# Kernel tuning notes

Hardware: AMD Instinct MI355X
Metric: run time of the kernel (lower is better)

The kernel has to match this reference:

```python
import jax, jax.numpy as jnp
import numpy as np

N = 100000   # nodes
E = 3200000  # edges (avg degree 32)
D = 768      # embedding_dim (XLM-R)
H = 256      # hidden_dim
L = 3        # num GCN layers
C = 3        # verdict classes


def setup_inputs() -> dict:
    key = jax.random.key(0)
    ks = jax.random.split(key, 8)
    s = 0.02
    return dict(
        node_features=jax.random.normal(ks[0], (N, D), jnp.float32),
        edge_src=jax.random.randint(ks[1], (E,), 0, N),
        edge_dst=jax.random.randint(ks[2], (E,), 0, N),
        claim_node_idx=0,
        W_in=(jax.random.normal(ks[3], (D, H), jnp.float32) * s),
        b_in=jnp.zeros((H,), jnp.float32),
        W_gnn=(jax.random.normal(ks[4], (L, H, H), jnp.float32) * s),
        b_gnn=jnp.zeros((L, H), jnp.float32),
        Wc1=(jax.random.normal(ks[5], (H, H // 2), jnp.float32) * s),
        bc1=jnp.zeros((H // 2,), jnp.float32),
        Wc2=(jax.random.normal(ks[6], (H // 2, C), jnp.float32) * s),
        bc2=jnp.zeros((C,), jnp.float32),
    )


def reference(node_features, edge_src, edge_dst, claim_node_idx,
              W_in, b_in, W_gnn, b_gnn, Wc1, bc1, Wc2, bc2):
    n = node_features.shape[0]
    dt = node_features.dtype
    ones = jnp.ones((edge_src.shape[0],), dt)
    # DGL GraphConv norm='both': symmetric normalization, degrees clamped >= 1
    deg_out = jnp.clip(jax.ops.segment_sum(ones, edge_src, num_segments=n), 1.0)
    deg_in = jnp.clip(jax.ops.segment_sum(ones, edge_dst, num_segments=n), 1.0)
    norm_src = deg_out ** -0.5  # [n]
    norm_dst = deg_in ** -0.5   # [n]

    # input projection
    h = node_features @ W_in + b_in  # [n, H]

    # GCN layers: relu(D_dst^-1/2 A D_src^-1/2 (h) W + b); dropout is identity in eval
    for l in range(W_gnn.shape[0]):
        msg = (h * norm_src[:, None])[edge_src]                      # [E, H] gather
        agg = jax.ops.segment_sum(msg, edge_dst, num_segments=n)     # [n, H] scatter-add
        agg = agg * norm_dst[:, None]
        h = jax.nn.relu(agg @ W_gnn[l] + b_gnn[l])

    claim = h[claim_node_idx]                       # [H]
    hid = jax.nn.relu(claim @ Wc1 + bc1)            # [H//2]
    logits = hid @ Wc2 + bc2                        # [C]
    return logits
```

## Files before the change

kernel.cpp:

```cpp
#include <hip/hip_runtime.h>
#include <hip/hip_bf16.h>

#define D_IN 768
#define H_DIM 256
#define H_HALF 128
#define N_CLASSES 3

#define CAP1 256
#define CAP2 16384
#define CAPDEG 128
#define CAP0 1024

typedef __attribute__((ext_vector_type(8))) short bf16x8;
typedef __attribute__((ext_vector_type(4))) float f32x4;

static __device__ __forceinline__ unsigned short f2bf(float f) {
    union { float f; unsigned u; } x; x.f = f;
    unsigned u = x.u;
    return (unsigned short)((u + 0x7FFFu + ((u >> 16) & 1u)) >> 16);
}
static __device__ __forceinline__ float bf2f(unsigned short b) {
    union { unsigned u; float f; } x; x.u = ((unsigned)b) << 16;
    return x.f;
}
static __device__ __forceinline__ float bflo(unsigned v) {
    union { unsigned u; float f; } x; x.u = v << 16;
    return x.f;
}
static __device__ __forceinline__ float bfhi(unsigned v) {
    union { unsigned u; float f; } x; x.u = v & 0xFFFF0000u;
    return x.f;
}
static __device__ __forceinline__ bool bit_test(const unsigned* __restrict__ bm, int i) {
    return (bm[i >> 5] >> (i & 31)) & 1u;
}

static __device__ __forceinline__ void try_append(int s, int* __restrict__ pos,
                                                  int* __restrict__ list, int* __restrict__ cnt,
                                                  unsigned* __restrict__ bmCur,
                                                  unsigned* __restrict__ bmL) {
    if (atomicCAS(&pos[s], -1, -2) == -1) {
        int i = atomicAdd(cnt, 1);
        list[i] = s;
        atomicOr(&bmCur[s >> 5], 1u << (s & 31));
        atomicOr(&bmL[s >> 5], 1u << (s & 31));
        atomicExch(&pos[s], i);
    }
}

__global__ void k_pass1(const int* __restrict__ src, const int* __restrict__ dst,
                        const int* __restrict__ claim, int* __restrict__ B0,
                        int* __restrict__ cur0, int* __restrict__ pos1,
                        int* __restrict__ list1, int* __restrict__ cnt1,
                        unsigned* __restrict__ bm1, unsigned* __restrict__ bmL,
                        const float* __restrict__ W_in, const float* __restrict__ W_gnn,
                        unsigned short* __restrict__ Wth_in, unsigned short* __restrict__ Wtl_in,
                        unsigned short* __restrict__ Wth_g, unsigned short* __restrict__ Wtl_g,
                        int E) {
    int idx = blockIdx.x * 256 + threadIdx.x;
    int nth = gridDim.x * 256;
    {
        const int n1 = D_IN * H_DIM;
        const int ntot = n1 + 2 * H_DIM * H_DIM;
        for (int id = idx; id < ntot; id += nth) {
            if (id < n1) {
                int k = id >> 8, n = id & 255;
                float w = W_in[id];
                unsigned short h = f2bf(w);
                Wth_in[(size_t)n * D_IN + k] = h;
                Wtl_in[(size_t)n * D_IN + k] = f2bf(w - bf2f(h));
            } else {
                int t = id - n1;
                int l = t >> 16, r = t & 65535;
                int k = r >> 8, n = r & 255;
                float w = W_gnn[(size_t)l * 65536 + r];
                unsigned short h = f2bf(w);
                Wth_g[(size_t)l * 65536 + (size_t)n * H_DIM + k] = h;
                Wtl_g[(size_t)l * 65536 + (size_t)n * H_DIM + k] = f2bf(w - bf2f(h));
            }
        }
    }
    int c = claim[0];
    int e0 = idx * 4;
    if (e0 >= E) return;
    if (e0 + 4 <= E) {
        int4 d4 = *(const int4*)(dst + e0);
#pragma unroll
        for (int k = 0; k < 4; k++) {
            int d = (k == 0) ? d4.x : (k == 1) ? d4.y : (k == 2) ? d4.z : d4.w;
            if (d == c) {
                int s = src[e0 + k];
                int p = atomicAdd(cur0, 1);
                if (p < CAP0) B0[p] = s;
                try_append(s, pos1, list1, cnt1, bm1, bmL);
            }
        }
    } else {
        for (int e = e0; e < E; e++) {
            int d = dst[e];
            if (d == c) {
                int s = src[e];
                int p = atomicAdd(cur0, 1);
                if (p < CAP0) B0[p] = s;
                try_append(s, pos1, list1, cnt1, bm1, bmL);
            }
        }
    }
}

__global__ void k_scan_bm(const int* __restrict__ dst, const unsigned* __restrict__ bmPrev,
                          unsigned char* __restrict__ mb, int E) {
    int idx = blockIdx.x * 256 + threadIdx.x;
    int e0 = idx * 4;
    if (e0 >= E) return;
    unsigned m = 0;
    if (e0 + 4 <= E) {
        int4 d4 = *(const int4*)(dst + e0);
        m  = bit_test(bmPrev, d4.x) ? 1u : 0u;
        m |= bit_test(bmPrev, d4.y) ? 2u : 0u;
        m |= bit_test(bmPrev, d4.z) ? 4u : 0u;
        m |= bit_test(bmPrev, d4.w) ? 8u : 0u;
    } else {
        for (int e = e0; e < E; e++)
            if (bit_test(bmPrev, dst[e])) m |= 1u << (e - e0);
    }
    mb[idx] = (unsigned char)m;
}

__global__ void k_xexpand(const unsigned char* __restrict__ mb, int nbytes,
                          const int* __restrict__ src, const int* __restrict__ dst,
                          const int* __restrict__ posPrev, int* __restrict__ bucket,
                          int* __restrict__ cur, int* __restrict__ posCur,
                          int* __restrict__ listCur, int* __restrict__ cntCur,
                          unsigned* __restrict__ bmCur, unsigned* __restrict__ bmL) {
    int i = blockIdx.x * 256 + threadIdx.x;
    int nwords = (nbytes + 3) / 4;
    if (i >= nwords) return;
    unsigned w = *(const unsigned*)(mb + (size_t)i * 4);
    int rem = nbytes - i * 4;
    if (rem < 4) w &= (1u << (rem * 8)) - 1u;
    if (!w) return;
    while (w) {
        int b = __ffs(w) - 1;
        w &= w - 1;
        int e = (i * 4 + (b >> 3)) * 4 + (b & 7);
        int s = src[e], d = dst[e];
        int pt = posPrev[d];
        int p = atomicAdd(&cur[pt], 1);
        if (p < CAPDEG) bucket[(size_t)pt * CAPDEG + p] = s;
        try_append(s, posCur, listCur, cntCur, bmCur, bmL);
    }
}

__global__ void k_deg(const int* __restrict__ src, const unsigned* __restrict__ bmL,
                      int* __restrict__ deg_out, int E) {
    int idx = blockIdx.x * 256 + threadIdx.x;
    int e0 = idx * 4;
    if (e0 >= E) return;
    if (e0 + 4 <= E) {
        int4 s4 = *(const int4*)(src + e0);
#pragma unroll
        for (int k = 0; k < 4; k++) {
            int s = (k == 0) ? s4.x : (k == 1) ? s4.y : (k == 2) ? s4.z : s4.w;
            if (bit_test(bmL, s)) atomicAdd(&deg_out[s], 1);
        }
    } else {
        for (int e = e0; e < E; e++) {
            int s = src[e];
            if (bit_test(bmL, s)) atomicAdd(&deg_out[s], 1);
        }
    }
}

template<bool GATHER_A, bool RELU, bool ALO, bool BLO>
__global__ __launch_bounds__(256) void k_mfma_gemm(
    const float* __restrict__ A, const int* __restrict__ rowmap,
    const int* __restrict__ Mptr,
    const unsigned short* __restrict__ Bth, const unsigned short* __restrict__ Btl,
    const float* __restrict__ bias, const int* __restrict__ deg_out,
    unsigned short* __restrict__ MsgOut, int K) {
    int M = Mptr[0];
    int row0 = blockIdx.x * 128;
    if (row0 >= M) return;
    int col0 = blockIdx.y * 128;

    __shared__ unsigned short Ash[128][40];
    __shared__ unsigned short Asl[ALO ? 128 : 1][40];
    __shared__ unsigned short Bsh[128][40];
    __shared__ unsigned short Bsl[BLO ? 128 : 1][40];

    int tid = threadIdx.x;
    int lane = tid & 63;
    int wv = tid >> 6;
    int wr = wv >> 1, wc = wv & 1;

    f32x4 acc[4][4];
#pragma unroll
    for (int mi = 0; mi < 4; mi++)
#pragma unroll
        for (int ni = 0; ni < 4; ni++) acc[mi][ni] = (f32x4){0.f, 0.f, 0.f, 0.f};

    int kf = (lane >> 4) * 8;
    int rsel = lane & 15;

    for (int kk = 0; kk < K; kk += 32) {
#pragma unroll
        for (int u = 0; u < 4; u++) {
            int i = tid + u * 256;
            int r = i >> 3;
            int c4 = (i & 7) * 4;
            float4 v = {0.f, 0.f, 0.f, 0.f};
            int row = row0 + r;
            if (row < M) {
                int arow = GATHER_A ? rowmap[row] : row;
                v = *(const float4*)(A + (size_t)arow * K + kk + c4);
            }
            ushort4 h;
            h.x = f2bf(v.x); h.y = f2bf(v.y); h.z = f2bf(v.z); h.w = f2bf(v.w);
            *(ushort4*)&Ash[r][c4] = h;
            if (ALO) {
                ushort4 l;
                l.x = f2bf(v.x - bf2f(h.x));
                l.y = f2bf(v.y - bf2f(h.y));
                l.z = f2bf(v.z - bf2f(h.z));
                l.w = f2bf(v.w - bf2f(h.w));
                *(ushort4*)&Asl[r][c4] = l;
            }
        }
#pragma unroll
        for (int u = 0; u < 2; u++) {
            int i = tid + u * 256;
            int r = i >> 2;
            int c8 = (i & 3) * 8;
            *(uint4*)&Bsh[r][c8] = *(const uint4*)(Bth + (size_t)(col0 + r) * K + kk + c8);
            if (BLO)
                *(uint4*)&Bsl[r][c8] = *(const uint4*)(Btl + (size_t)(col0 + r) * K + kk + c8);
        }
        __syncthreads();

        bf16x8 ah[4], al[4], bh[4], bl[4];
#pragma unroll
        for (int mi = 0; mi < 4; mi++) {
            ah[mi] = *(const bf16x8*)&Ash[wr * 64 + mi * 16 + rsel][kf];
            if (ALO) al[mi] = *(const bf16x8*)&Asl[wr * 64 + mi * 16 + rsel][kf];
        }
#pragma unroll
        for (int ni = 0; ni < 4; ni++) {
            bh[ni] = *(const bf16x8*)&Bsh[wc * 64 + ni * 16 + rsel][kf];
            if (BLO) bl[ni] = *(const bf16x8*)&Bsl[wc * 64 + ni * 16 + rsel][kf];
        }
#pragma unroll
        for (int mi = 0; mi < 4; mi++)
#pragma unroll
            for (int ni = 0; ni < 4; ni++) {
                acc[mi][ni] = __builtin_amdgcn_mfma_f32_16x16x32_bf16(ah[mi], bh[ni], acc[mi][ni], 0, 0, 0);
                if (ALO)
                    acc[mi][ni] = __builtin_amdgcn_mfma_f32_16x16x32_bf16(al[mi], bh[ni], acc[mi][ni], 0, 0, 0);
                if (BLO)
                    acc[mi][ni] = __builtin_amdgcn_mfma_f32_16x16x32_bf16(ah[mi], bl[ni], acc[mi][ni], 0, 0, 0);
            }
        __syncthreads();
    }

    int lr = (lane >> 4) * 4;
    int lc = lane & 15;
    float bcol[4];
#pragma unroll
    for (int ni = 0; ni < 4; ni++) bcol[ni] = bias[col0 + wc * 64 + ni * 16 + lc];

#pragma unroll
    for (int mi = 0; mi < 4; mi++) {
#pragma unroll
        for (int r = 0; r < 4; r++) {
            int row = row0 + wr * 64 + mi * 16 + lr + r;
            if (row >= M) continue;
            float ns = rsqrtf((float)max(deg_out[rowmap[row]], 1));
#pragma unroll
            for (int ni = 0; ni < 4; ni++) {
                int col = col0 + wc * 64 + ni * 16 + lc;
                float v = acc[mi][ni][r] + bcol[ni];
                if (RELU) v = fmaxf(v, 0.f);
                MsgOut[(size_t)row * 256 + col] = f2bf(v * ns);
            }
        }
    }
}

__global__ void k_gather_agg(const int* __restrict__ nTptr, const int* __restrict__ bucket,
                             const int* __restrict__ cur, const int* __restrict__ posSrc,
                             const uint2* __restrict__ Msg, float4* __restrict__ Agg) {
    int nT = nTptr[0];
    int gt = blockIdx.x * blockDim.x + threadIdx.x;
    int w = gt >> 6, lane = gt & 63;
    if (w >= nT) return;
    int deg = cur[w];
    int ne = min(deg, CAPDEG);
    const int* bk = bucket + (size_t)w * CAPDEG;
    float a0 = 0.f, a1 = 0.f, a2 = 0.f, a3 = 0.f;
    int e = 0;
    for (; e + 1 < ne; e += 2) {
        int s0 = __builtin_amdgcn_readfirstlane(bk[e]);
        int s1 = __builtin_amdgcn_readfirstlane(bk[e + 1]);
        int i0 = __builtin_amdgcn_readfirstlane(posSrc[s0]);
        int i1 = __builtin_amdgcn_readfirstlane(posSrc[s1]);
        uint2 v0 = Msg[(size_t)i0 * 64 + lane];
        uint2 v1 = Msg[(size_t)i1 * 64 + lane];
        a0 += bflo(v0.x) + bflo(v1.x);
        a1 += bfhi(v0.x) + bfhi(v1.x);
        a2 += bflo(v0.y) + bflo(v1.y);
        a3 += bfhi(v0.y) + bfhi(v1.y);
    }
    for (; e < ne; e++) {
        int s = __builtin_amdgcn_readfirstlane(bk[e]);
        int i0 = __builtin_amdgcn_readfirstlane(posSrc[s]);
        uint2 v = Msg[(size_t)i0 * 64 + lane];
        a0 += bflo(v.x); a1 += bfhi(v.x); a2 += bflo(v.y); a3 += bfhi(v.y);
    }
    float nd = rsqrtf((float)max(deg, 1));
    float4 o;
    o.x = a0 * nd; o.y = a1 * nd; o.z = a2 * nd; o.w = a3 * nd;
    Agg[(size_t)w * 64 + lane] = o;
}

__global__ void k_final(const int* __restrict__ B0, const int* __restrict__ cur0,
                        const int* __restrict__ pos1, const unsigned short* __restrict__ Msg2,
                        const float* __restrict__ W3, const float* __restrict__ b3,
                        const float* __restrict__ Wc1, const float* __restrict__ bc1,
                        const float* __restrict__ Wc2, const float* __restrict__ bc2,
                        float* __restrict__ out) {
    __shared__ float agg[H_DIM];
    __shared__ float h3[H_DIM];
    __shared__ float hid[H_HALF];
    int t = threadIdx.x;
    int deg = cur0[0];
    int ne = min(deg, CAP0);
    float a = 0.f;
    for (int e = 0; e < ne; e++) {
        int s = B0[e];
        int idx = pos1[s];
        a += bf2f(Msg2[(size_t)idx * H_DIM + t]);
    }
    agg[t] = a * rsqrtf((float)max(deg, 1));
    __syncthreads();
    float acc = b3[t];
    for (int k = 0; k < H_DIM; k++) acc += agg[k] * W3[k * H_DIM + t];
    h3[t] = fmaxf(acc, 0.f);
    __syncthreads();
    if (t < H_HALF) {
        float x = bc1[t];
        for (int k = 0; k < H_DIM; k++) x += h3[k] * Wc1[k * H_HALF + t];
        hid[t] = fmaxf(x, 0.f);
    }
    __syncthreads();
    if (t < N_CLASSES) {
        float x = bc2[t];
        for (int j = 0; j < H_HALF; j++) x += hid[j] * Wc2[j * N_CLASSES + t];
        out[t] = x;
    }
}

extern "C" void kernel_launch(void* const* d_in, const int* in_sizes, int n_in,
                              void* d_out, int out_size, void* d_ws, size_t ws_size,
                              hipStream_t stream) {
    const float* nf    = (const float*)d_in[0];
    const int*   esrc  = (const int*)d_in[1];
    const int*   edst  = (const int*)d_in[2];
    const int*   claim = (const int*)d_in[3];
    const float* W_in  = (const float*)d_in[4];
    const float* b_in  = (const float*)d_in[5];
    const float* W_gnn = (const float*)d_in[6];
    const float* b_gnn = (const float*)d_in[7];
    const float* Wc1   = (const float*)d_in[8];
    const float* bc1   = (const float*)d_in[9];
    const float* Wc2   = (const float*)d_in[10];
    const float* bc2   = (const float*)d_in[11];

    const int N = in_sizes[0] / D_IN;
    const int E = in_sizes[1];
    const int BMWP = (((N + 31) / 32) + 63) & ~63;
    const int NBYTES = (E + 3) / 4;

    char* p = (char*)d_ws;
    auto alloc = [&](size_t bytes) -> void* {
        void* r = (void*)p;
        p += (bytes + 255) & ~(size_t)255;
        return r;
    };
    char* zero0 = p;
    int* deg_out  = (int*)alloc((size_t)N * 4);
    unsigned* bms = (unsigned*)alloc((size_t)3 * BMWP * 4);
    int* cnt      = (int*)alloc(8 * 4);
    int* cur1     = (int*)alloc((size_t)CAP1 * 4);
    int* cur2     = (int*)alloc((size_t)CAP2 * 4);
    size_t zeroBytes = (size_t)(p - zero0);
    char* ff0 = p;
    int* pos1     = (int*)alloc((size_t)N * 4);
    int* pos2     = (int*)alloc((size_t)N * 4);
    int* pos3     = (int*)alloc((size_t)N * 4);
    size_t ffBytes = (size_t)(p - ff0);
    unsigned* bm1 = bms;
    unsigned* bm2 = bms + BMWP;
    unsigned* bmL = bms + 2 * BMWP;
    int* list1    = (int*)alloc((size_t)CAP1 * 4);
    int* list2    = (int*)alloc((size_t)CAP2 * 4);
    int* list3    = (int*)alloc((size_t)N * 4);
    int* B0       = (int*)alloc((size_t)CAP0 * 4);
    int* B1       = (int*)alloc((size_t)CAP1 * CAPDEG * 4);
    int* B2       = (int*)alloc((size_t)CAP2 * CAPDEG * 4);
    unsigned char* mb = (unsigned char*)alloc((size_t)NBYTES + 8);
    unsigned short* Wth_in = (unsigned short*)alloc((size_t)D_IN * H_DIM * 2);
    unsigned short* Wtl_in = (unsigned short*)alloc((size_t)D_IN * H_DIM * 2);
    unsigned short* Wth_g  = (unsigned short*)alloc((size_t)2 * H_DIM * H_DIM * 2);
    unsigned short* Wtl_g  = (unsigned short*)alloc((size_t)2 * H_DIM * H_DIM * 2);
    unsigned short* Msg0 = (unsigned short*)alloc((size_t)N * H_DIM * 2);
    unsigned short* Msg1 = (unsigned short*)alloc((size_t)CAP2 * H_DIM * 2);
    unsigned short* Msg2 = (unsigned short*)alloc((size_t)CAP1 * H_DIM * 2);
    float* Agg1 = (float*)alloc((size_t)CAP2 * H_DIM * 4);
    float* Agg2 = (float*)alloc((size_t)CAP1 * H_DIM * 4);

    hipMemsetAsync(zero0, 0, zeroBytes, stream);
    hipMemsetAsync(ff0, 0xFF, ffBytes, stream);

    int e4b = ((E + 3) / 4 + 255) / 256;
    int exb = (((NBYTES + 3) / 4) + 255) / 256;

    k_pass1<<<e4b, 256, 0, stream>>>(esrc, edst, claim, B0, cnt + 3, pos1, list1, cnt,
                                     bm1, bmL, W_in, W_gnn, Wth_in, Wtl_in, Wth_g, Wtl_g, E);
    k_scan_bm<<<e4b, 256, 0, stream>>>(edst, bm1, mb, E);
    k_xexpand<<<exb, 256, 0, stream>>>(mb, NBYTES, esrc, edst, pos1, B1, cur1,
                                       pos2, list2, cnt + 1, bm2, bmL);
    k_scan_bm<<<e4b, 256, 0, stream>>>(edst, bm2, mb, E);
    k_xexpand<<<exb, 256, 0, stream>>>(mb, NBYTES, esrc, edst, pos2, B2, cur2,
                                       pos3, list3, cnt + 2, bmL, bmL);
    k_deg<<<e4b, 256, 0, stream>>>(esrc, bmL, deg_out, E);

    dim3 gproj((N + 127) / 128, 2);
    k_mfma_gemm<true, false, false, false><<<gproj, 256, 0, stream>>>(
        nf, list3, cnt + 2, Wth_in, Wtl_in, b_in, deg_out, Msg0, D_IN);

    k_gather_agg<<<(CAP2 * 64 + 255) / 256, 256, 0, stream>>>(cnt + 1, B2, cur2, pos3,
                                                              (const uint2*)Msg0, (float4*)Agg1);
    dim3 g1(CAP2 / 128, 2);
    k_mfma_gemm<false, true, true, true><<<g1, 256, 0, stream>>>(
        Agg1, list2, cnt + 1, Wth_g, Wtl_g, b_gnn, deg_out, Msg1, H_DIM);

    k_gather_agg<<<(CAP1 * 64 + 255) / 256, 256, 0, stream>>>(cnt, B1, cur1, pos2,
                                                              (const uint2*)Msg1, (float4*)Agg2);
    dim3 g2(CAP1 / 128, 2);
    k_mfma_gemm<false, true, true, true><<<g2, 256, 0, stream>>>(
        Agg2, list1, cnt, Wth_g + (size_t)H_DIM * H_DIM, Wtl_g + (size_t)H_DIM * H_DIM,
        b_gnn + H_DIM, deg_out, Msg2, H_DIM);

    k_final<<<1, H_DIM, 0, stream>>>(B0, cnt + 3, pos1, Msg2,
                                     W_gnn + (size_t)2 * H_DIM * H_DIM, b_gnn + 2 * H_DIM,
                                     Wc1, bc1, Wc2, bc2, (float*)d_out);
}
```

Baseline: 338.6 us.

## Fuse edge bitmap scan and frontier expansion into one kernel, 8 edges per thread

The separate bitmap-scan and expand kernels are merged into one kernel. Each block builds its 2048-edge match mask in shared memory, then 64 threads walk the set bits and append matching edges to the frontier buckets. This drops the global mask buffer and two kernel launches per hop. The pass1 and degree kernels now also handle 8 edges per thread with two int4 loads, halving their grid size. In exchange, only a quarter of each block's threads do the expansion step, and the weight-conversion work folded into pass1 now runs on fewer threads.

```diff
diff --git a/kernel.cpp b/kernel.cpp
--- a/kernel.cpp
+++ b/kernel.cpp
@@ -81,14 +81,15 @@
         }
     }
     int c = claim[0];
-    int e0 = idx * 4;
+    int e0 = idx * 8;
     if (e0 >= E) return;
-    if (e0 + 4 <= E) {
-        int4 d4 = *(const int4*)(dst + e0);
-#pragma unroll
-        for (int k = 0; k < 4; k++) {
-            int d = (k == 0) ? d4.x : (k == 1) ? d4.y : (k == 2) ? d4.z : d4.w;
-            if (d == c) {
+    if (e0 + 8 <= E) {
+        int4 da = *(const int4*)(dst + e0);
+        int4 db = *(const int4*)(dst + e0 + 4);
+        int ds[8] = {da.x, da.y, da.z, da.w, db.x, db.y, db.z, db.w};
+#pragma unroll
+        for (int k = 0; k < 8; k++) {
+            if (ds[k] == c) {
                 int s = src[e0 + k];
                 int p = atomicAdd(cur0, 1);
                 if (p < CAP0) B0[p] = s;
@@ -97,8 +98,7 @@
         }
     } else {
         for (int e = e0; e < E; e++) {
-            int d = dst[e];
-            if (d == c) {
+            if (dst[e] == c) {
                 int s = src[e];
                 int p = atomicAdd(cur0, 1);
                 if (p < CAP0) B0[p] = s;
@@ -108,42 +108,40 @@
     }
 }
 
-__global__ void k_scan_bm(const int* __restrict__ dst, const unsigned* __restrict__ bmPrev,
-                          unsigned char* __restrict__ mb, int E) {
-    int idx = blockIdx.x * 256 + threadIdx.x;
-    int e0 = idx * 4;
-    if (e0 >= E) return;
+__global__ void k_scan_expand(const int* __restrict__ src, const int* __restrict__ dst,
+                              const unsigned* __restrict__ bmPrev, const int* __restrict__ posPrev,
+                              int* __restrict__ bucket, int* __restrict__ cur,
+                              int* __restrict__ posCur, int* __restrict__ listCur,
+                              int* __restrict__ cntCur,
+                              unsigned* __restrict__ bmCur, unsigned* __restrict__ bmL, int E) {
+    __shared__ unsigned mwords[64];
+    int tid = threadIdx.x;
+    int e0 = blockIdx.x * 2048 + tid * 8;
     unsigned m = 0;
-    if (e0 + 4 <= E) {
-        int4 d4 = *(const int4*)(dst + e0);
-        m  = bit_test(bmPrev, d4.x) ? 1u : 0u;
-        m |= bit_test(bmPrev, d4.y) ? 2u : 0u;
-        m |= bit_test(bmPrev, d4.z) ? 4u : 0u;
-        m |= bit_test(bmPrev, d4.w) ? 8u : 0u;
+    if (e0 + 8 <= E) {
+        int4 da = *(const int4*)(dst + e0);
+        int4 db = *(const int4*)(dst + e0 + 4);
+        m  = bit_test(bmPrev, da.x) ? 1u : 0u;
+        m |= bit_test(bmPrev, da.y) ? 2u : 0u;
+        m |= bit_test(bmPrev, da.z) ? 4u : 0u;
+        m |= bit_test(bmPrev, da.w) ? 8u : 0u;
+        m |= bit_test(bmPrev, db.x) ? 16u : 0u;
+        m |= bit_test(bmPrev, db.y) ? 32u : 0u;
+        m |= bit_test(bmPrev, db.z) ? 64u : 0u;
+        m |= bit_test(bmPrev, db.w) ? 128u : 0u;
     } else {
         for (int e = e0; e < E; e++)
             if (bit_test(bmPrev, dst[e])) m |= 1u << (e - e0);
     }
-    mb[idx] = (unsigned char)m;
-}
-
-__global__ void k_xexpand(const unsigned char* __restrict__ mb, int nbytes,
-                          const int* __restrict__ src, const int* __restrict__ dst,
-                          const int* __restrict__ posPrev, int* __restrict__ bucket,
-                          int* __restrict__ cur, int* __restrict__ posCur,
-                          int* __restrict__ listCur, int* __restrict__ cntCur,
-                          unsigned* __restrict__ bmCur, unsigned* __restrict__ bmL) {
-    int i = blockIdx.x * 256 + threadIdx.x;
-    int nwords = (nbytes + 3) / 4;
-    if (i >= nwords) return;
-    unsigned w = *(const unsigned*)(mb + (size_t)i * 4);
-    int rem = nbytes - i * 4;
-    if (rem < 4) w &= (1u << (rem * 8)) - 1u;
-    if (!w) return;
+    ((unsigned char*)mwords)[tid] = (unsigned char)m;
+    __syncthreads();
+    if (tid >= 64) return;
+    unsigned w = mwords[tid];
+    int base = blockIdx.x * 2048 + tid * 32;
     while (w) {
         int b = __ffs(w) - 1;
         w &= w - 1;
-        int e = (i * 4 + (b >> 3)) * 4 + (b & 7);
+        int e = base + (b >> 3) * 8 + (b & 7);
         int s = src[e], d = dst[e];
         int pt = posPrev[d];
         int p = atomicAdd(&cur[pt], 1);
@@ -155,15 +153,15 @@
 __global__ void k_deg(const int* __restrict__ src, const unsigned* __restrict__ bmL,
                       int* __restrict__ deg_out, int E) {
     int idx = blockIdx.x * 256 + threadIdx.x;
-    int e0 = idx * 4;
+    int e0 = idx * 8;
     if (e0 >= E) return;
-    if (e0 + 4 <= E) {
-        int4 s4 = *(const int4*)(src + e0);
-#pragma unroll
-        for (int k = 0; k < 4; k++) {
-            int s = (k == 0) ? s4.x : (k == 1) ? s4.y : (k == 2) ? s4.z : s4.w;
-            if (bit_test(bmL, s)) atomicAdd(&deg_out[s], 1);
-        }
+    if (e0 + 8 <= E) {
+        int4 a = *(const int4*)(src + e0);
+        int4 b = *(const int4*)(src + e0 + 4);
+        int ss[8] = {a.x, a.y, a.z, a.w, b.x, b.y, b.z, b.w};
+#pragma unroll
+        for (int k = 0; k < 8; k++)
+            if (bit_test(bmL, ss[k])) atomicAdd(&deg_out[ss[k]], 1);
     } else {
         for (int e = e0; e < E; e++) {
             int s = src[e];
@@ -378,7 +376,6 @@
     const int N = in_sizes[0] / D_IN;
     const int E = in_sizes[1];
     const int BMWP = (((N + 31) / 32) + 63) & ~63;
-    const int NBYTES = (E + 3) / 4;
 
     char* p = (char*)d_ws;
     auto alloc = [&](size_t bytes) -> void* {
@@ -407,7 +404,6 @@
     int* B0       = (int*)alloc((size_t)CAP0 * 4);
     int* B1       = (int*)alloc((size_t)CAP1 * CAPDEG * 4);
     int* B2       = (int*)alloc((size_t)CAP2 * CAPDEG * 4);
-    unsigned char* mb = (unsigned char*)alloc((size_t)NBYTES + 8);
     unsigned short* Wth_in = (unsigned short*)alloc((size_t)D_IN * H_DIM * 2);
     unsigned short* Wtl_in = (unsigned short*)alloc((size_t)D_IN * H_DIM * 2);
     unsigned short* Wth_g  = (unsigned short*)alloc((size_t)2 * H_DIM * H_DIM * 2);
@@ -421,18 +417,15 @@
     hipMemsetAsync(zero0, 0, zeroBytes, stream);
     hipMemsetAsync(ff0, 0xFF, ffBytes, stream);
 
-    int e4b = ((E + 3) / 4 + 255) / 256;
-    int exb = (((NBYTES + 3) / 4) + 255) / 256;
-
-    k_pass1<<<e4b, 256, 0, stream>>>(esrc, edst, claim, B0, cnt + 3, pos1, list1, cnt,
+    int e8b = (E + 2047) / 2048;
+
+    k_pass1<<<e8b, 256, 0, stream>>>(esrc, edst, claim, B0, cnt + 3, pos1, list1, cnt,
                                      bm1, bmL, W_in, W_gnn, Wth_in, Wtl_in, Wth_g, Wtl_g, E);
-    k_scan_bm<<<e4b, 256, 0, stream>>>(edst, bm1, mb, E);
-    k_xexpand<<<exb, 256, 0, stream>>>(mb, NBYTES, esrc, edst, pos1, B1, cur1,
-                                       pos2, list2, cnt + 1, bm2, bmL);
-    k_scan_bm<<<e4b, 256, 0, stream>>>(edst, bm2, mb, E);
-    k_xexpand<<<exb, 256, 0, stream>>>(mb, NBYTES, esrc, edst, pos2, B2, cur2,
-                                       pos3, list3, cnt + 2, bmL, bmL);
-    k_deg<<<e4b, 256, 0, stream>>>(esrc, bmL, deg_out, E);
+    k_scan_expand<<<e8b, 256, 0, stream>>>(esrc, edst, bm1, pos1, B1, cur1,
+                                           pos2, list2, cnt + 1, bm2, bmL, E);
+    k_scan_expand<<<e8b, 256, 0, stream>>>(esrc, edst, bm2, pos2, B2, cur2,
+                                           pos3, list3, cnt + 2, bmL, bmL, E);
+    k_deg<<<e8b, 256, 0, stream>>>(esrc, bmL, deg_out, E);
 
     dim3 gproj((N + 127) / 128, 2);
     k_mfma_gemm<true, false, false, false><<<gproj, 256, 0, stream>>>(
```

After: 310.6 us. 1.09x faster.
